# Kernel tuning notes

Hardware: AMD Instinct MI355X
Metric: run time of the kernel (lower is better)

Reference implementation:

```python
import jax, jax.numpy as jnp
import numpy as np

NEG_SLOPE = 0.2  # PyG GATv2Conv default leaky_relu slope
N_NODES = 50000
N_EDGES = 800000
F_IN = 128
HID = 32
HEADS = 4
OUT_HEADS = 1
N_CLS = 16
MLP_HID = 128


def topk_mask(score, dst, k, num_nodes):
    """Boolean mask [E,H]: True where edge score is among top-k for its destination."""
    E = score.shape[0]
    counts = jnp.zeros((num_nodes,), jnp.int32).at[dst].add(1)
    starts = jnp.cumsum(counts) - counts  # first sorted index of each dst segment

    def one_head(s):
        o1 = jnp.argsort(-s)                       # sort by score desc
        o2 = jnp.argsort(dst[o1], stable=True)     # stable sort by dst -> (dst asc, score desc)
        perm = o1[o2]
        rank = jnp.arange(E) - starts[dst[perm]]   # rank within dst segment
        return jnp.zeros((E,), bool).at[perm].set(rank < k)

    return jax.vmap(one_head, in_axes=1, out_axes=1)(score)


def masked_segment_softmax(score, mask, dst, num_nodes):
    neg = jnp.where(mask, score, -jnp.inf)
    m = jax.ops.segment_max(neg, dst, num_segments=num_nodes)
    m = jnp.where(jnp.isfinite(m), m, 0.0)
    ex = jnp.where(mask, jnp.exp(score - m[dst]), 0.0)
    s = jax.ops.segment_sum(ex, dst, num_segments=num_nodes)
    return ex / (s[dst] + 1e-16)


def gatv2_topk(x, edge_index, k, Wl, Wr, att, b, heads, out_c, concat, num_nodes):
    src, dst = edge_index[0], edge_index[1]
    xl = (x @ Wl).reshape(num_nodes, heads, out_c)
    xr = (x @ Wr).reshape(num_nodes, heads, out_c)
    h = xl[src] + xr[dst]                                   # [E,H,C]
    e = jnp.einsum('ehc,hc->eh', jax.nn.leaky_relu(h, NEG_SLOPE), att)  # [E,H]
    keep = topk_mask(e, dst, k, num_nodes)
    alpha = masked_segment_softmax(e, keep, dst, num_nodes)       # top-k attention
    alpha_n = masked_segment_softmax(e, ~keep, dst, num_nodes)    # truncated (noise) attention
    msg = xl[src]                                                  # [E,H,C]
    out = jax.ops.segment_sum(alpha[..., None] * msg, dst, num_segments=num_nodes)
    noise = jax.ops.segment_sum(alpha_n[..., None] * msg, dst, num_segments=num_nodes)
    if concat:
        out = out.reshape(num_nodes, heads * out_c)
        noise = noise.reshape(num_nodes, heads * out_c)
    else:
        out = out.mean(axis=1)
        noise = noise.mean(axis=1)
    return out + b, noise + b


def setup_inputs() -> dict:
    key = jax.random.key(0)
    ks = jax.random.split(key, 14)
    s = 0.1
    x = jax.random.normal(ks[0], (N_NODES, F_IN), jnp.float32)
    edge_index = jax.random.randint(ks[1], (2, N_EDGES), 0, N_NODES, dtype=jnp.int64)
    return {
        'x': x,
        'edge_index': edge_index,
        'attn_topk': 8,
        'Wl1': jax.random.normal(ks[2], (F_IN, HEADS * HID), jnp.float32) * s,
        'Wr1': jax.random.normal(ks[3], (F_IN, HEADS * HID), jnp.float32) * s,
        'att1': jax.random.normal(ks[4], (HEADS, HID), jnp.float32) * s,
        'b1': jnp.zeros((HEADS * HID,), jnp.float32),
        'Wl2': jax.random.normal(ks[5], (HEADS * HID, OUT_HEADS * N_CLS), jnp.float32) * s,
        'Wr2': jax.random.normal(ks[6], (HEADS * HID, OUT_HEADS * N_CLS), jnp.float32) * s,
        'att2': jax.random.normal(ks[7], (OUT_HEADS, N_CLS), jnp.float32) * s,
        'b2': jnp.zeros((N_CLS,), jnp.float32),
        'lin1_w': jax.random.normal(ks[8], (HEADS * HID, MLP_HID), jnp.float32) * s,
        'lin1_b': jnp.zeros((MLP_HID,), jnp.float32),
        'lin2_w': jax.random.normal(ks[9], (MLP_HID, N_CLS), jnp.float32) * s,
        'lin2_b': jnp.zeros((N_CLS,), jnp.float32),
    }


def reference(x, edge_index, attn_topk, Wl1, Wr1, att1, b1, Wl2, Wr2, att2, b2,
              lin1_w, lin1_b, lin2_w, lin2_b):
    # eval mode: dropout is identity
    h, noise1 = gatv2_topk(x, edge_index, attn_topk, Wl1, Wr1, att1, b1,
                           HEADS, HID, True, N_NODES)
    h = jax.nn.elu(h)
    n1 = jax.nn.elu(noise1 @ lin1_w + lin1_b) @ lin2_w + lin2_b
    out, noise2 = gatv2_topk(h, edge_index, attn_topk, Wl2, Wr2, att2, b2,
                             OUT_HEADS, N_CLS, False, N_NODES)
    return (jax.nn.log_softmax(out, axis=1),
            jax.nn.log_softmax(n1, axis=1),
            jax.nn.log_softmax(noise2, axis=1))
```

## Files before the change

kernel.cpp:

```cpp
#include <hip/hip_runtime.h>
#include <math.h>

#define NN 50000
#define NE 800000
#define FIN 128
#define HEADS 4
#define HID 32
#define D1 128
#define NCLS 16
#define NEG 0.2f
#define NINF (-3.402823466e38f)
#define CAP 64
#define SB 256
#define NSB ((NN + SB - 1) / SB)

__global__ void k_count(const int* __restrict__ dst, int* __restrict__ counts) {
  int j = blockIdx.x * 256 + threadIdx.x;
  if (j < NE) atomicAdd(&counts[dst[j]], 1);
}

__global__ void k_scanA(const int* __restrict__ counts, int* __restrict__ bsum) {
  int b = blockIdx.x, t = threadIdx.x;
  int idx = b * SB + t;
  int v = idx < NN ? counts[idx] : 0;
  __shared__ int ws[4];
#pragma unroll
  for (int o = 1; o <= 32; o <<= 1) v += __shfl_xor(v, o, 64);
  if ((t & 63) == 0) ws[t >> 6] = v;
  __syncthreads();
  if (t == 0) bsum[b] = ws[0] + ws[1] + ws[2] + ws[3];
}

__global__ void k_scanB(const int* __restrict__ bsum, int* __restrict__ boff) {
  int t = threadIdx.x;
  int v = t < NSB ? bsum[t] : 0;
  __shared__ int tmp[256];
  tmp[t] = v;
  __syncthreads();
  for (int o = 1; o < 256; o <<= 1) {
    int u = t >= o ? tmp[t - o] : 0;
    __syncthreads();
    tmp[t] += u;
    __syncthreads();
  }
  if (t < NSB) boff[t] = tmp[t] - v;
}

__global__ void k_scanC(const int* __restrict__ counts, const int* __restrict__ boff,
                        int* __restrict__ starts, int* __restrict__ cursor) {
  int b = blockIdx.x, t = threadIdx.x;
  int idx = b * SB + t;
  int v = idx < NN ? counts[idx] : 0;
  __shared__ int tmp[256];
  tmp[t] = v;
  __syncthreads();
  for (int o = 1; o < 256; o <<= 1) {
    int u = t >= o ? tmp[t - o] : 0;
    __syncthreads();
    tmp[t] += u;
    __syncthreads();
  }
  int ex = tmp[t] - v + boff[b];
  if (idx < NN) { starts[idx] = ex; cursor[idx] = ex; }
}

__global__ void k_scatter(const int* __restrict__ src, const int* __restrict__ dst,
                          int* __restrict__ cursor, int* __restrict__ eperm,
                          int* __restrict__ sperm) {
  int j = blockIdx.x * 256 + threadIdx.x;
  if (j < NE) {
    int p = atomicAdd(&cursor[dst[j]], 1);
    eperm[p] = j;
    sperm[p] = src[j];
  }
}

template <int BM, int BN, int BK, int TM, int TN, int ACT>
__global__ __launch_bounds__(256) void k_gemm2(
    const float* __restrict__ A, const float* __restrict__ B1,
    const float* __restrict__ B2, int N1, int s1, int s2,
    const float* __restrict__ bias, float* __restrict__ C, int M, int N, int K) {
  constexpr int NT = (BM / TM) * (BN / TN);
  static_assert(NT == 256, "block must be 256 threads");
  static_assert(TM % 4 == 0 && TN % 4 == 0, "float4 fragments");
  __shared__ float As[BK][BM + 4];
  __shared__ float Bs[BK][BN];
  int tid = threadIdx.x;
  int bm = blockIdx.y * BM, bn = blockIdx.x * BN;
  constexpr int TX = BN / TN;
  int tn = (tid % TX) * TN;
  int tm = (tid / TX) * TM;
  float acc[TM][TN];
#pragma unroll
  for (int i = 0; i < TM; i++)
#pragma unroll
    for (int j = 0; j < TN; j++) acc[i][j] = 0.f;

  for (int k0 = 0; k0 < K; k0 += BK) {
    constexpr int AV = BM * BK / 4;
    for (int i = tid; i < AV; i += NT) {
      int r = i / (BK / 4);
      int c4 = (i % (BK / 4)) * 4;
      float4 v = make_float4(0.f, 0.f, 0.f, 0.f);
      int gr = bm + r;
      if (gr < M) v = *(const float4*)(A + (size_t)gr * K + k0 + c4);
      As[c4 + 0][r] = v.x; As[c4 + 1][r] = v.y; As[c4 + 2][r] = v.z; As[c4 + 3][r] = v.w;
    }
    constexpr int BV = BK * BN / 4;
    for (int i = tid; i < BV; i += NT) {
      int r = i / (BN / 4), c4 = (i % (BN / 4)) * 4;
      int gc = bn + c4, gk = k0 + r;
      float4 v = (gc < N1) ? *(const float4*)(B1 + (size_t)gk * s1 + gc)
                           : *(const float4*)(B2 + (size_t)gk * s2 + (gc - N1));
      Bs[r][c4 + 0] = v.x; Bs[r][c4 + 1] = v.y; Bs[r][c4 + 2] = v.z; Bs[r][c4 + 3] = v.w;
    }
    __syncthreads();
#pragma unroll
    for (int kk = 0; kk < BK; kk++) {
      float ra[TM], rb[TN];
#pragma unroll
      for (int i = 0; i < TM; i += 4)
        *(float4*)&ra[i] = *(const float4*)&As[kk][tm + i];
#pragma unroll
      for (int j = 0; j < TN; j += 4)
        *(float4*)&rb[j] = *(const float4*)&Bs[kk][tn + j];
#pragma unroll
      for (int i = 0; i < TM; i++)
#pragma unroll
        for (int j = 0; j < TN; j++) acc[i][j] += ra[i] * rb[j];
    }
    __syncthreads();
  }
#pragma unroll
  for (int i = 0; i < TM; i++) {
    int gr = bm + tm + i;
    if (gr >= M) continue;
#pragma unroll
    for (int j = 0; j < TN; j += 4) {
      float4 v;
      v.x = acc[i][j + 0]; v.y = acc[i][j + 1]; v.z = acc[i][j + 2]; v.w = acc[i][j + 3];
      if (bias) {
        v.x += bias[bn + tn + j + 0]; v.y += bias[bn + tn + j + 1];
        v.z += bias[bn + tn + j + 2]; v.w += bias[bn + tn + j + 3];
      }
      if (ACT == 1) {
        v.x = v.x > 0.f ? v.x : expm1f(v.x);
        v.y = v.y > 0.f ? v.y : expm1f(v.y);
        v.z = v.z > 0.f ? v.z : expm1f(v.z);
        v.w = v.w > 0.f ? v.w : expm1f(v.w);
      }
      *(float4*)(C + (size_t)gr * N + bn + tn + j) = v;
    }
  }
}

__device__ __forceinline__ bool lex_gt(float av, int ai, float bv, int bi) {
  return (av > bv) || (av == bv && ai < bi);
}

__global__ __launch_bounds__(256) void k_fused1(
    const float* __restrict__ xlr, const float* __restrict__ att,
    const int* __restrict__ sperm, const int* __restrict__ eperm,
    const int* __restrict__ starts, const int* __restrict__ counts,
    const int* __restrict__ kptr, const float* __restrict__ bias,
    float* __restrict__ hout, float* __restrict__ nout) {
  __shared__ float sc[4][CAP][4];
  int w = threadIdx.x >> 6;
  int l = threadIdx.x & 63;
  int d = blockIdx.x * 4 + w;
  if (d >= NN) return;
  int st = starts[d];
  int deg = counts[d];
  if (deg > CAP) deg = CAP;
  int k = kptr[0];

  int srcreg = 0, idreg = 0x7fffffff;
  if (l < deg) { srcreg = sperm[st + l]; idreg = eperm[st + l]; }

  int h2 = l >> 5, li = l & 31;
  int headq = li >> 3;
  float4 xrv = *(const float4*)(xlr + (size_t)d * 256 + 128 + 4 * li);
  float4 attv = *(const float4*)(att + 4 * li);
  float4 b1v = *(const float4*)(bias + 4 * li);

  for (int q = 0; q < deg; q += 8) {
    int rr[4]; int ssr[4]; bool vv[4]; float4 xv[4]; float pp[4];
#pragma unroll
    for (int j = 0; j < 4; j++) {
      rr[j] = q + 2 * j + h2;
      ssr[j] = __shfl(srcreg, rr[j]);
      vv[j] = rr[j] < deg;
      xv[j] = make_float4(0.f, 0.f, 0.f, 0.f);
      if (vv[j]) xv[j] = *(const float4*)(xlr + (size_t)ssr[j] * 256 + 4 * li);
    }
#pragma unroll
    for (int j = 0; j < 4; j++) {
      float a, p = 0.f;
      a = xv[j].x + xrv.x; p += fmaxf(a, NEG * a) * attv.x;
      a = xv[j].y + xrv.y; p += fmaxf(a, NEG * a) * attv.y;
      a = xv[j].z + xrv.z; p += fmaxf(a, NEG * a) * attv.z;
      a = xv[j].w + xrv.w; p += fmaxf(a, NEG * a) * attv.w;
      pp[j] = p;
    }
#pragma unroll
    for (int o = 1; o <= 4; o <<= 1) {
#pragma unroll
      for (int j = 0; j < 4; j++) pp[j] += __shfl_xor(pp[j], o, 64);
    }
    if ((li & 7) == 0) {
#pragma unroll
      for (int j = 0; j < 4; j++)
        if (vv[j]) sc[w][rr[j]][headq] = pp[j];
    }
  }

  int hh = l >> 4, ii = l & 15;
  float sv[4]; int si[4]; int rank[4]; bool val[4];
#pragma unroll
  for (int j = 0; j < 4; j++) {
    int q = j * 16 + ii;
    val[j] = q < deg;
    sv[j] = val[j] ? sc[w][q][hh] : NINF;
    int bid = __shfl(idreg, q);
    si[j] = val[j] ? bid : 0x7fffffff;
    rank[j] = 0;
  }
#pragma unroll
  for (int ch = 0; ch < 4; ch++) {
    if (ch * 16 >= deg) break;
#pragma unroll
    for (int pp = 0; pp < 16; pp++) {
      int p = ch * 16 + pp;
      float bv = __shfl(sv[ch], hh * 16 + pp);
      int bi = __shfl(si[ch], hh * 16 + pp);
      if (p < deg) {
#pragma unroll
        for (int j = 0; j < 4; j++) rank[j] += lex_gt(bv, bi, sv[j], si[j]);
      }
    }
  }
  bool kept[4];
#pragma unroll
  for (int j = 0; j < 4; j++) kept[j] = val[j] && (rank[j] < k);
  float mk = fmaxf(fmaxf(sv[0], sv[1]), fmaxf(sv[2], sv[3]));
  float mn = NINF;
#pragma unroll
  for (int j = 0; j < 4; j++) mn = fmaxf(mn, kept[j] ? NINF : sv[j]);
#pragma unroll
  for (int o = 1; o <= 8; o <<= 1) {
    mk = fmaxf(mk, __shfl_xor(mk, o, 64));
    mn = fmaxf(mn, __shfl_xor(mn, o, 64));
  }
  float ek[4], en[4], sk = 0.f, sn = 0.f;
#pragma unroll
  for (int j = 0; j < 4; j++) {
    ek[j] = kept[j] ? __expf(sv[j] - mk) : 0.f;
    en[j] = (val[j] && !kept[j]) ? __expf(sv[j] - mn) : 0.f;
    sk += ek[j]; sn += en[j];
  }
#pragma unroll
  for (int o = 1; o <= 8; o <<= 1) {
    sk += __shfl_xor(sk, o, 64);
    sn += __shfl_xor(sn, o, 64);
  }
  float ik = 1.f / (sk + 1e-16f), inn = 1.f / (sn + 1e-16f);
#pragma unroll
  for (int j = 0; j < 4; j++) {
    if (val[j]) sc[w][j * 16 + ii][hh] = kept[j] ? ek[j] * ik : -(en[j] * inn);
  }

  float4 ao = make_float4(0.f, 0.f, 0.f, 0.f), an = ao;
  for (int q = 0; q < deg; q += 4) {
    int r0 = q + h2, r1 = q + 2 + h2;
    int s0 = __shfl(srcreg, r0), s1 = __shfl(srcreg, r1);
    if (r0 < deg) {
      float wv = sc[w][r0][headq];
      float pw = fmaxf(wv, 0.f), nw = pw - wv;
      float4 xv = *(const float4*)(xlr + (size_t)s0 * 256 + 4 * li);
      ao.x += pw * xv.x; ao.y += pw * xv.y; ao.z += pw * xv.z; ao.w += pw * xv.w;
      an.x += nw * xv.x; an.y += nw * xv.y; an.z += nw * xv.z; an.w += nw * xv.w;
    }
    if (r1 < deg) {
      float wv = sc[w][r1][headq];
      float pw = fmaxf(wv, 0.f), nw = pw - wv;
      float4 xv = *(const float4*)(xlr + (size_t)s1 * 256 + 4 * li);
      ao.x += pw * xv.x; ao.y += pw * xv.y; ao.z += pw * xv.z; ao.w += pw * xv.w;
      an.x += nw * xv.x; an.y += nw * xv.y; an.z += nw * xv.z; an.w += nw * xv.w;
    }
  }
  ao.x += __shfl_xor(ao.x, 32, 64); ao.y += __shfl_xor(ao.y, 32, 64);
  ao.z += __shfl_xor(ao.z, 32, 64); ao.w += __shfl_xor(ao.w, 32, 64);
  an.x += __shfl_xor(an.x, 32, 64); an.y += __shfl_xor(an.y, 32, 64);
  an.z += __shfl_xor(an.z, 32, 64); an.w += __shfl_xor(an.w, 32, 64);
  if (h2 == 0) {
    float4 vo;
    vo.x = ao.x + b1v.x; vo.y = ao.y + b1v.y; vo.z = ao.z + b1v.z; vo.w = ao.w + b1v.w;
    vo.x = vo.x > 0.f ? vo.x : expm1f(vo.x);
    vo.y = vo.y > 0.f ? vo.y : expm1f(vo.y);
    vo.z = vo.z > 0.f ? vo.z : expm1f(vo.z);
    vo.w = vo.w > 0.f ? vo.w : expm1f(vo.w);
    *(float4*)(hout + (size_t)d * D1 + 4 * li) = vo;
  } else {
    float4 vn;
    vn.x = an.x + b1v.x; vn.y = an.y + b1v.y; vn.z = an.z + b1v.z; vn.w = an.w + b1v.w;
    *(float4*)(nout + (size_t)d * D1 + 4 * li) = vn;
  }
}

__global__ __launch_bounds__(256) void k_fused2(
    const float* __restrict__ xlr, const float* __restrict__ att,
    const int* __restrict__ sperm, const int* __restrict__ eperm,
    const int* __restrict__ starts, const int* __restrict__ counts,
    const int* __restrict__ kptr, const float* __restrict__ bias,
    float* __restrict__ out0, float* __restrict__ out1) {
  __shared__ float sc[4][CAP];
  int w = threadIdx.x >> 6;
  int l = threadIdx.x & 63;
  int d = blockIdx.x * 4 + w;
  if (d >= NN) return;
  int st = starts[d];
  int deg = counts[d];
  if (deg > CAP) deg = CAP;
  int k = kptr[0];

  int srcreg = 0, idreg = 0x7fffffff;
  if (l < deg) { srcreg = sperm[st + l]; idreg = eperm[st + l]; }

  int g = l >> 4, li = l & 15;
  float xrv = xlr[(size_t)d * 32 + 16 + li];
  float attv = att[li];
  float bv2 = bias[li];

  for (int q = 0; q < deg; q += 8) {
    int r0 = q + g, r1 = q + 4 + g;
    int s0 = __shfl(srcreg, r0), s1 = __shfl(srcreg, r1);
    float x0 = (r0 < deg) ? xlr[(size_t)s0 * 32 + li] : 0.f;
    float x1 = (r1 < deg) ? xlr[(size_t)s1 * 32 + li] : 0.f;
    float a0 = x0 + xrv, a1 = x1 + xrv;
    float p0 = fmaxf(a0, NEG * a0) * attv;
    float p1 = fmaxf(a1, NEG * a1) * attv;
#pragma unroll
    for (int o = 1; o <= 8; o <<= 1) {
      p0 += __shfl_xor(p0, o, 64);
      p1 += __shfl_xor(p1, o, 64);
    }
    if (li == 0) {
      if (r0 < deg) sc[w][r0] = p0;
      if (r1 < deg) sc[w][r1] = p1;
    }
  }

  float sv = (l < deg) ? sc[w][l] : NINF;
  int si = idreg;
  int rank = 0;
  for (int p = 0; p < deg; p++) {
    float bv = __shfl(sv, p);
    int bi = __shfl(si, p);
    rank += lex_gt(bv, bi, sv, si);
  }
  bool kept = (l < deg) && (rank < k);
  float mk = sv, mn = kept ? NINF : sv;
#pragma unroll
  for (int o = 1; o <= 32; o <<= 1) {
    mk = fmaxf(mk, __shfl_xor(mk, o, 64));
    mn = fmaxf(mn, __shfl_xor(mn, o, 64));
  }
  float ek = kept ? __expf(sv - mk) : 0.f;
  float en = ((l < deg) && !kept) ? __expf(sv - mn) : 0.f;
  float sk = ek, sn = en;
#pragma unroll
  for (int o = 1; o <= 32; o <<= 1) {
    sk += __shfl_xor(sk, o, 64);
    sn += __shfl_xor(sn, o, 64);
  }
  if (l < deg) sc[w][l] = kept ? ek / (sk + 1e-16f) : -(en / (sn + 1e-16f));

  float ao = 0.f, an = 0.f;
  for (int q = 0; q < deg; q += 4) {
    int r = q + g;
    int s = __shfl(srcreg, r);
    if (r < deg) {
      float wv = sc[w][r];
      float pw = fmaxf(wv, 0.f), nw = pw - wv;
      float xv = xlr[(size_t)s * 32 + li];
      ao += pw * xv; an += nw * xv;
    }
  }
  ao += __shfl_xor(ao, 16, 64); ao += __shfl_xor(ao, 32, 64);
  an += __shfl_xor(an, 16, 64); an += __shfl_xor(an, 32, 64);
  float vo = ao + bv2, vn = an + bv2;
  float mo = vo, mv = vn;
#pragma unroll
  for (int o = 1; o <= 8; o <<= 1) {
    mo = fmaxf(mo, __shfl_xor(mo, o, 64));
    mv = fmaxf(mv, __shfl_xor(mv, o, 64));
  }
  float eo = __expf(vo - mo), ev = __expf(vn - mv);
#pragma unroll
  for (int o = 1; o <= 8; o <<= 1) {
    eo += __shfl_xor(eo, o, 64);
    ev += __shfl_xor(ev, o, 64);
  }
  if (g == 0) out0[(size_t)d * NCLS + li] = vo - (mo + logf(eo));
  if (g == 1) out1[(size_t)d * NCLS + li] = vn - (mv + logf(ev));
}

__global__ void k_lsm(const float* __restrict__ in, float* __restrict__ out) {
  int r = blockIdx.x * 256 + threadIdx.x;
  if (r >= NN) return;
  const float4* p = (const float4*)(in + (size_t)r * NCLS);
  float4 a = p[0], b = p[1], c = p[2], d4 = p[3];
  float vals[16] = {a.x, a.y, a.z, a.w, b.x, b.y, b.z, b.w,
                    c.x, c.y, c.z, c.w, d4.x, d4.y, d4.z, d4.w};
  float m = vals[0];
#pragma unroll
  for (int i = 1; i < 16; i++) m = fmaxf(m, vals[i]);
  float s = 0.f;
#pragma unroll
  for (int i = 0; i < 16; i++) s += expf(vals[i] - m);
  float l = m + logf(s);
  float* op = out + (size_t)r * NCLS;
#pragma unroll
  for (int i = 0; i < 16; i++) op[i] = vals[i] - l;
}

extern "C" void kernel_launch(void* const* d_in, const int* in_sizes, int n_in,
                              void* d_out, int out_size, void* d_ws, size_t ws_size,
                              hipStream_t stream) {
  (void)in_sizes; (void)n_in; (void)out_size; (void)ws_size;
  const float* x    = (const float*)d_in[0];
  const int*   ei   = (const int*)d_in[1];
  const int*   kptr = (const int*)d_in[2];
  const float* Wl1  = (const float*)d_in[3];
  const float* Wr1  = (const float*)d_in[4];
  const float* att1 = (const float*)d_in[5];
  const float* b1   = (const float*)d_in[6];
  const float* Wl2  = (const float*)d_in[7];
  const float* Wr2  = (const float*)d_in[8];
  const float* att2 = (const float*)d_in[9];
  const float* b2   = (const float*)d_in[10];
  const float* l1w  = (const float*)d_in[11];
  const float* l1b  = (const float*)d_in[12];
  const float* l2w  = (const float*)d_in[13];
  const float* l2b  = (const float*)d_in[14];
  const int* srcv = ei;
  const int* dstv = ei + NE;

  char* wp = (char*)d_ws;
  auto alloc = [&](size_t n) { char* p = wp; wp += (n + 255) & ~(size_t)255; return p; };
  float* xlr1   = (float*)alloc((size_t)NN * 256 * 4);
  float* hbuf   = (float*)alloc((size_t)NN * D1 * 4);
  float* noise1 = (float*)alloc((size_t)NN * D1 * 4);
  float* t1     = (float*)alloc((size_t)NN * D1 * 4);
  float* xlr2   = (float*)alloc((size_t)NN * 32 * 4);
  float* n1buf  = (float*)alloc((size_t)NN * NCLS * 4);
  int* counts = (int*)alloc((size_t)NN * 4);
  int* starts = (int*)alloc((size_t)NN * 4);
  int* cursor = (int*)alloc((size_t)NN * 4);
  int* eperm  = (int*)alloc((size_t)NE * 4);
  int* sperm  = (int*)alloc((size_t)NE * 4);
  int* bsum   = (int*)alloc((size_t)NSB * 4);
  int* boff   = (int*)alloc((size_t)NSB * 4);

  hipMemsetAsync(counts, 0, (size_t)NN * 4, stream);
  k_count<<<(NE + 255) / 256, 256, 0, stream>>>(dstv, counts);
  k_scanA<<<NSB, 256, 0, stream>>>(counts, bsum);
  k_scanB<<<1, 256, 0, stream>>>(bsum, boff);
  k_scanC<<<NSB, 256, 0, stream>>>(counts, boff, starts, cursor);
  k_scatter<<<(NE + 255) / 256, 256, 0, stream>>>(srcv, dstv, cursor, eperm, sperm);

  k_gemm2<64, 128, 32, 4, 8, 0><<<dim3(2, (NN + 63) / 64), 256, 0, stream>>>(
      x, Wl1, Wr1, 128, 128, 128, nullptr, xlr1, NN, 256, FIN);

  k_fused1<<<(NN + 3) / 4, 256, 0, stream>>>(xlr1, att1, sperm, eperm,
                                             starts, counts, kptr, b1, hbuf, noise1);

  k_gemm2<64, 128, 32, 4, 8, 1><<<dim3(1, (NN + 63) / 64), 256, 0, stream>>>(
      noise1, l1w, l1w, 128, 128, 128, l1b, t1, NN, 128, 128);
  k_gemm2<256, 16, 32, 4, 4, 0><<<dim3(1, (NN + 255) / 256), 256, 0, stream>>>(
      t1, l2w, l2w, 16, 16, 16, l2b, n1buf, NN, NCLS, 128);

  k_gemm2<128, 32, 32, 4, 4, 0><<<dim3(1, (NN + 127) / 128), 256, 0, stream>>>(
      hbuf, Wl2, Wr2, 16, 16, 16, nullptr, xlr2, NN, 32, D1);

  float* o = (float*)d_out;
  k_fused2<<<(NN + 3) / 4, 256, 0, stream>>>(xlr2, att2, sperm, eperm, starts,
                                             counts, kptr, b2, o,
                                             o + (size_t)2 * NN * NCLS);

  k_lsm<<<(NN + 255) / 256, 256, 0, stream>>>(n1buf, o + (size_t)NN * NCLS);
}
```

Baseline: 488.6 us.

## Cache gathered source features in registers for aggregation and enlarge GEMM tiles

In both fused GAT kernels, the source feature vectors gathered during score computation for the first 16 (layer 1) or 32 (layer 2) edges are now held in registers. The aggregation pass reuses them instead of gathering them from global memory a second time, and only higher-degree nodes fall back to re-gathering. Separately, the two 128-wide GEMMs switch from 64-row to 128-row tiles with 8x8 per-thread micro-tiles. The register cache and the larger micro-tiles raise register pressure, which may lower occupancy.

New measurement: 512.1 us. 4.8% more time.

```diff
diff --git a/kernel.cpp b/kernel.cpp
--- a/kernel.cpp
+++ b/kernel.cpp
@@ -183,15 +183,53 @@
   float4 attv = *(const float4*)(att + 4 * li);
   float4 b1v = *(const float4*)(bias + 4 * li);
 
-  for (int q = 0; q < deg; q += 8) {
-    int rr[4]; int ssr[4]; bool vv[4]; float4 xv[4]; float pp[4];
+  float4 xc[8];
+#pragma unroll
+  for (int j = 0; j < 8; j++) xc[j] = make_float4(0.f, 0.f, 0.f, 0.f);
+
+#pragma unroll
+  for (int Q = 0; Q < 16; Q += 8) {
+    if (Q < deg) {
+      int rr[4]; float4 xv[4]; float pp[4]; bool vv[4];
+#pragma unroll
+      for (int j = 0; j < 4; j++) {
+        rr[j] = Q + 2 * j + h2;
+        int s = __shfl(srcreg, rr[j]);
+        vv[j] = rr[j] < deg;
+        xv[j] = make_float4(0.f, 0.f, 0.f, 0.f);
+        if (vv[j]) xv[j] = *(const float4*)(xlr + (size_t)s * 256 + 4 * li);
+        xc[Q / 2 + j] = xv[j];
+      }
+#pragma unroll
+      for (int j = 0; j < 4; j++) {
+        float a, p = 0.f;
+        a = xv[j].x + xrv.x; p += fmaxf(a, NEG * a) * attv.x;
+        a = xv[j].y + xrv.y; p += fmaxf(a, NEG * a) * attv.y;
+        a = xv[j].z + xrv.z; p += fmaxf(a, NEG * a) * attv.z;
+        a = xv[j].w + xrv.w; p += fmaxf(a, NEG * a) * attv.w;
+        pp[j] = p;
+      }
+#pragma unroll
+      for (int o = 1; o <= 4; o <<= 1) {
+#pragma unroll
+        for (int j = 0; j < 4; j++) pp[j] += __shfl_xor(pp[j], o, 64);
+      }
+      if ((li & 7) == 0) {
+#pragma unroll
+        for (int j = 0; j < 4; j++)
+          if (vv[j]) sc[w][rr[j]][headq] = pp[j];
+      }
+    }
+  }
+  for (int q = 16; q < deg; q += 8) {
+    int rr[4]; float4 xv[4]; float pp[4]; bool vv[4];
 #pragma unroll
     for (int j = 0; j < 4; j++) {
       rr[j] = q + 2 * j + h2;
-      ssr[j] = __shfl(srcreg, rr[j]);
+      int s = __shfl(srcreg, rr[j]);
       vv[j] = rr[j] < deg;
       xv[j] = make_float4(0.f, 0.f, 0.f, 0.f);
-      if (vv[j]) xv[j] = *(const float4*)(xlr + (size_t)ssr[j] * 256 + 4 * li);
+      if (vv[j]) xv[j] = *(const float4*)(xlr + (size_t)s * 256 + 4 * li);
     }
 #pragma unroll
     for (int j = 0; j < 4; j++) {
@@ -270,7 +308,18 @@
   }
 
   float4 ao = make_float4(0.f, 0.f, 0.f, 0.f), an = ao;
-  for (int q = 0; q < deg; q += 4) {
+#pragma unroll
+  for (int j = 0; j < 8; j++) {
+    int r = 2 * j + h2;
+    if (r < deg) {
+      float wv = sc[w][r][headq];
+      float pw = fmaxf(wv, 0.f), nw = pw - wv;
+      float4 xv = xc[j];
+      ao.x += pw * xv.x; ao.y += pw * xv.y; ao.z += pw * xv.z; ao.w += pw * xv.w;
+      an.x += nw * xv.x; an.y += nw * xv.y; an.z += nw * xv.z; an.w += nw * xv.w;
+    }
+  }
+  for (int q = 16; q < deg; q += 4) {
     int r0 = q + h2, r1 = q + 2 + h2;
     int s0 = __shfl(srcreg, r0), s1 = __shfl(srcreg, r1);
     if (r0 < deg) {
@@ -331,7 +380,33 @@
   float attv = att[li];
   float bv2 = bias[li];
 
-  for (int q = 0; q < deg; q += 8) {
+  float xc[8];
+#pragma unroll
+  for (int j = 0; j < 8; j++) xc[j] = 0.f;
+
+#pragma unroll
+  for (int Q = 0; Q < 32; Q += 8) {
+    if (Q < deg) {
+      int r0 = Q + g, r1 = Q + 4 + g;
+      int s0 = __shfl(srcreg, r0), s1 = __shfl(srcreg, r1);
+      float x0 = (r0 < deg) ? xlr[(size_t)s0 * 32 + li] : 0.f;
+      float x1 = (r1 < deg) ? xlr[(size_t)s1 * 32 + li] : 0.f;
+      xc[Q / 4] = x0; xc[Q / 4 + 1] = x1;
+      float a0 = x0 + xrv, a1 = x1 + xrv;
+      float p0 = fmaxf(a0, NEG * a0) * attv;
+      float p1 = fmaxf(a1, NEG * a1) * attv;
+#pragma unroll
+      for (int o = 1; o <= 8; o <<= 1) {
+        p0 += __shfl_xor(p0, o, 64);
+        p1 += __shfl_xor(p1, o, 64);
+      }
+      if (li == 0) {
+        if (r0 < deg) sc[w][r0] = p0;
+        if (r1 < deg) sc[w][r1] = p1;
+      }
+    }
+  }
+  for (int q = 32; q < deg; q += 8) {
     int r0 = q + g, r1 = q + 4 + g;
     int s0 = __shfl(srcreg, r0), s1 = __shfl(srcreg, r1);
     float x0 = (r0 < deg) ? xlr[(size_t)s0 * 32 + li] : 0.f;
@@ -376,7 +451,16 @@
   if (l < deg) sc[w][l] = kept ? ek / (sk + 1e-16f) : -(en / (sn + 1e-16f));
 
   float ao = 0.f, an = 0.f;
-  for (int q = 0; q < deg; q += 4) {
+#pragma unroll
+  for (int j = 0; j < 8; j++) {
+    int r = 4 * j + g;
+    if (r < deg) {
+      float wv = sc[w][r];
+      float pw = fmaxf(wv, 0.f), nw = pw - wv;
+      ao += pw * xc[j]; an += nw * xc[j];
+    }
+  }
+  for (int q = 32; q < deg; q += 4) {
     int r = q + g;
     int s = __shfl(srcreg, r);
     if (r < deg) {
@@ -469,13 +553,13 @@
   k_scanC<<<NSB, 256, 0, stream>>>(counts, boff, starts, cursor);
   k_scatter<<<(NE + 255) / 256, 256, 0, stream>>>(srcv, dstv, cursor, eperm, sperm);
 
-  k_gemm2<64, 128, 32, 4, 8, 0><<<dim3(2, (NN + 63) / 64), 256, 0, stream>>>(
+  k_gemm2<128, 128, 32, 8, 8, 0><<<dim3(2, (NN + 127) / 128), 256, 0, stream>>>(
       x, Wl1, Wr1, 128, 128, 128, nullptr, xlr1, NN, 256, FIN);
 
   k_fused1<<<(NN + 3) / 4, 256, 0, stream>>>(xlr1, att1, sperm, eperm,
                                              starts, counts, kptr, b1, hbuf, noise1);
 
-  k_gemm2<64, 128, 32, 4, 8, 1><<<dim3(1, (NN + 63) / 64), 256, 0, stream>>>(
+  k_gemm2<128, 128, 32, 8, 8, 1><<<dim3(1, (NN + 127) / 128), 256, 0, stream>>>(
       noise1, l1w, l1w, 128, 128, 128, l1b, t1, NN, 128, 128);
   k_gemm2<256, 16, 32, 4, 4, 0><<<dim3(1, (NN + 255) / 256), 256, 0, stream>>>(
       t1, l2w, l2w, 16, 16, 16, l2b, n1buf, NN, NCLS, 128);
```
